# Kernel optimization log

Measured on AMD Instinct MI355X. Metric: run time of the kernel, lower is better.

## Reference

```python
import jax, jax.numpy as jnp
import numpy as np

S, B, L = 64, 32, 64          # seq_len (messages), batch (convs), max tokens per message
V, D = 32000, 300             # vocab, embedding dim
H = 512                       # hidden_dim; per-direction message hidden = H//2
F = 16                        # num_game_features
Hh = H // 2


def lstm_dir(x, mask, Wih, Whh, b, reverse=False):
    """Masked (packed-equivalent) LSTM. x:(T,N,D), mask:(T,N) bool.
    Returns h:(T,N,H) with zeros at invalid steps (matches pad_packed_sequence)."""
    if reverse:
        x, mask = x[::-1], mask[::-1]
    N = x.shape[1]
    Hd = Whh.shape[1]
    xg = jnp.einsum('tnd,gd->tng', x, Wih) + b  # (T,N,4H) input gates precomputed

    def step(carry, inp):
        h, c = carry
        xg_t, m = inp
        g = xg_t + h @ Whh.T
        i, f, gg, o = jnp.split(g, 4, axis=-1)
        c_new = jax.nn.sigmoid(f) * c + jax.nn.sigmoid(i) * jnp.tanh(gg)
        h_new = jax.nn.sigmoid(o) * jnp.tanh(c_new)
        m = m[:, None]
        return (jnp.where(m, h_new, h), jnp.where(m, c_new, c)), jnp.where(m, h_new, 0.0)

    init = (jnp.zeros((N, Hd), x.dtype), jnp.zeros((N, Hd), x.dtype))
    _, hs = jax.lax.scan(step, init, (xg, mask))
    if reverse:
        hs = hs[::-1]
    return hs


def setup_inputs() -> dict:
    key = jax.random.key(0)
    ks = jax.random.split(key, 16)
    s = 1.0 / np.sqrt(Hh)
    sc = 1.0 / np.sqrt(H)
    inp = {
        'messages': jax.random.randint(ks[0], (S, B, L), 0, V),
        'game_features': jax.random.normal(ks[1], (S, B, F), jnp.float32),
        'conv_lengths': jax.random.randint(ks[2], (B,), 1, S + 1),
        'E': jax.random.normal(ks[3], (V, D), jnp.float32) * 0.1,  # frozen embedding
        # message bi-LSTM (forward dir)
        'Wih_f': jax.random.uniform(ks[4], (4 * Hh, D), jnp.float32, -s, s),
        'Whh_f': jax.random.uniform(ks[5], (4 * Hh, Hh), jnp.float32, -s, s),
        'b_f': jax.random.uniform(ks[6], (4 * Hh,), jnp.float32, -s, s),
        # message bi-LSTM (backward dir)
        'Wih_b': jax.random.uniform(ks[7], (4 * Hh, D), jnp.float32, -s, s),
        'Whh_b': jax.random.uniform(ks[8], (4 * Hh, Hh), jnp.float32, -s, s),
        'b_b': jax.random.uniform(ks[9], (4 * Hh,), jnp.float32, -s, s),
        # conversation LSTM
        'Wih_c': jax.random.uniform(ks[10], (4 * H, H), jnp.float32, -sc, sc),
        'Whh_c': jax.random.uniform(ks[11], (4 * H, H), jnp.float32, -sc, sc),
        'b_c': jax.random.uniform(ks[12], (4 * H,), jnp.float32, -sc, sc),
        # classifier
        'Wc': jax.random.uniform(ks[13], (H + F,), jnp.float32, -sc, sc),
        'bc': jax.random.uniform(ks[14], (), jnp.float32, -sc, sc),
    }
    return inp


def reference(messages, game_features, conv_lengths, E, Wih_f, Whh_f, b_f,
              Wih_b, Whh_b, b_b, Wih_c, Whh_c, b_c, Wc, bc):
    # ---- message level: all S*B messages in one batched bi-LSTM pass ----
    flat = messages.reshape(S * B, L)                       # (N, L)
    emb = E[flat]                                           # (N, L, D)
    msg_len = jnp.maximum((flat != 0).sum(1), 1)            # clamp(min=1)
    tmask = jnp.arange(L)[:, None] < msg_len[None, :]       # (L, N)
    x = emb.transpose(1, 0, 2)                              # (L, N, D) time-major
    h_fwd = lstm_dir(x, tmask, Wih_f, Whh_f, b_f, reverse=False)
    h_bwd = lstm_dir(x, tmask, Wih_b, Whh_b, b_b, reverse=True)
    h = jnp.concatenate([h_fwd, h_bwd], axis=-1)            # (L, N, H); zeros at pad
    enc = h.max(axis=0)                                     # maxpool incl. zero pads (torch semantics)
    enc = enc.reshape(S, B, H)
    # ---- conversation level ----
    cmask = jnp.arange(S)[:, None] < conv_lengths[None, :]  # (S, B)
    conv_out = lstm_dir(enc, cmask, Wih_c, Whh_c, b_c)      # (S, B, H), zeros past length
    # dropout is identity at inference
    combined = jnp.concatenate([conv_out, game_features], axis=2)  # (S, B, H+F)
    logits = combined @ Wc + bc                             # (S, B)
    return logits
```

## Files before the change

### kernel.cpp

```cpp
#include <hip/hip_runtime.h>
#include <cmath>

#define S_DIM 64
#define B_DIM 32
#define L_DIM 64
#define NMSG  2048
#define D_DIM 300
#define HH    256
#define HC    512
#define F_DIM 16
#define VOCAB 32000

#define OFF_XGV   0u
#define OFF_WHH   32768000u
#define OFF_WPI   33030144u
#define OFF_WCI   33357824u
#define OFF_WCR   33882112u
#define OFF_ENCB  34406400u
#define OFF_HCONV 34930688u
#define OFF_CCONV 34938880u
#define OFF_CO    34955264u
#define OFF_MLEN  36003840u

typedef __attribute__((ext_vector_type(8))) short s8v;
typedef __attribute__((ext_vector_type(4))) float f4v;
#define MFMA(a,b,c) __builtin_amdgcn_mfma_f32_16x16x32_bf16((a),(b),(c),0,0,0)

__device__ __forceinline__ unsigned short f2bf(float x) {
    unsigned u = __float_as_uint(x);
    return (unsigned short)((u + 0x7FFFu + ((u >> 16) & 1u)) >> 16);
}
__device__ __forceinline__ float bf2f(unsigned short u) {
    return __uint_as_float(((unsigned)u) << 16);
}
__device__ __forceinline__ float sigm(float x) { return 1.0f / (1.0f + __expf(-x)); }
__device__ __forceinline__ float tanh_f(float x) { return 1.0f - 2.0f / (1.0f + __expf(2.0f * x)); }

__device__ __forceinline__ void gload16(const unsigned short* g, unsigned short* l) {
    __builtin_amdgcn_global_load_lds(
        (const __attribute__((address_space(1))) unsigned int*)g,
        (__attribute__((address_space(3))) unsigned int*)l, 16, 0, 0);
}

__global__ __launch_bounds__(256) void pack_whh(
    const float* __restrict__ Whh_f, const float* __restrict__ Whh_b,
    unsigned short* __restrict__ Wp)
{
    int nt = blockIdx.x, dir = blockIdx.y;
    const float* W = dir ? Whh_b : Whh_f;
    int tid = threadIdx.x, lane = tid & 63, ktq = tid >> 6;
    int n = nt * 16 + (lane & 15);
    int kb = (lane >> 4) * 8;
    #pragma unroll
    for (int pass = 0; pass < 2; ++pass) {
        int kt = ktq + pass * 4;
        int k0 = kt * 32 + kb;
        unsigned short tmp[8];
        #pragma unroll
        for (int u = 0; u < 8; ++u) tmp[u] = f2bf(W[(size_t)n * HH + k0 + u]);
        *(uint4*)(Wp + (size_t)dir * 262144 + ((size_t)(nt * 8 + kt)) * 512 + lane * 8) = *(uint4*)tmp;
    }
}

__global__ __launch_bounds__(256) void pack_wih(
    const float* __restrict__ Wih_f, const float* __restrict__ Wih_b,
    unsigned short* __restrict__ wpi)
{
    int nt = blockIdx.x, dir = blockIdx.y;
    const float* W = dir ? Wih_b : Wih_f;
    int tid = threadIdx.x, lane = tid & 63, ktq = tid >> 6;
    int n = nt * 16 + (lane & 15);
    int kb = (lane >> 4) * 8;
    for (int kt = ktq; kt < 10; kt += 4) {
        int k0 = kt * 32 + kb;
        unsigned short tmp[8];
        #pragma unroll
        for (int u = 0; u < 8; ++u) {
            int k = k0 + u;
            tmp[u] = (k < D_DIM) ? f2bf(W[(size_t)n * D_DIM + k]) : (unsigned short)0;
        }
        *(uint4*)(wpi + (size_t)dir * 327680 + ((size_t)(nt * 10 + kt)) * 512 + lane * 8) = *(uint4*)tmp;
    }
}

__global__ __launch_bounds__(256) void pack_whc(
    const float* __restrict__ Wih_c, const float* __restrict__ Whh_c,
    unsigned short* __restrict__ whci, unsigned short* __restrict__ whcr)
{
    int nt = blockIdx.x, which = blockIdx.y;
    const float* W = which ? Whh_c : Wih_c;
    unsigned short* dst = which ? whcr : whci;
    int tid = threadIdx.x, lane = tid & 63;
    int row = nt * 16 + (lane & 15);
    int kb = (lane >> 4) * 8;
    for (int kt = tid >> 6; kt < 16; kt += 4) {
        int k0 = kt * 32 + kb;
        unsigned short tmp[8];
        #pragma unroll
        for (int u = 0; u < 8; ++u) tmp[u] = f2bf(W[(size_t)row * HC + k0 + u]);
        *(uint4*)(dst + ((size_t)(nt * 16 + kt)) * 512 + lane * 8) = *(uint4*)tmp;
    }
}

__global__ __launch_bounds__(256) void msg_len_kernel(const int* __restrict__ msgs,
                                                      int* __restrict__ mlen) {
    int n = blockIdx.x * 256 + threadIdx.x;
    if (n >= NMSG) return;
    int cnt = 0;
    #pragma unroll 8
    for (int l = 0; l < L_DIM; ++l) cnt += (msgs[n * L_DIM + l] != 0);
    mlen[n] = max(cnt, 1);
}

__global__ __launch_bounds__(256) void init_conv(float* __restrict__ ws) {
    unsigned i = blockIdx.x * 256u + threadIdx.x;
    if (i < 24576u) ws[OFF_HCONV + i] = 0.0f;
}

#define EROW 328
__global__ __launch_bounds__(256) void xg_gemm(
    const float* __restrict__ E,
    const float* __restrict__ b_f, const float* __restrict__ b_b,
    const unsigned short* __restrict__ wpi,
    unsigned short* __restrict__ xgv)
{
    __shared__ __align__(16) unsigned short e_lds[32 * EROW];
    __shared__ __align__(16) float gbuf[32 * 264];
    const int w0 = blockIdx.x * 32;
    const int n0 = blockIdx.y * 256;
    const int dirb = n0 >> 10;
    const int nb = n0 & 1023;
    const float* bias = dirb ? b_b : b_f;

    const int tid = threadIdx.x, lane = tid & 63, wv = tid >> 6;
    const int l15 = lane & 15, kg = lane >> 4;

    for (int i = tid; i < 32 * 320; i += 256) {
        int r = i / 320, k = i - r * 320;
        float v = (k < D_DIM) ? E[(size_t)(w0 + r) * D_DIM + k] : 0.0f;
        e_lds[r * EROW + k] = f2bf(v);
    }
    __syncthreads();

    const unsigned short* wb = wpi + (size_t)dirb * 327680;
    const f4v zf = {0.0f, 0.0f, 0.0f, 0.0f};
    f4v acc[2][4];
    #pragma unroll
    for (int m = 0; m < 2; ++m)
        #pragma unroll
        for (int q = 0; q < 4; ++q) acc[m][q] = zf;

    for (int kt = 0; kt < 10; ++kt) {
        s8v a0 = *(const s8v*)&e_lds[l15 * EROW + kt * 32 + kg * 8];
        s8v a1 = *(const s8v*)&e_lds[(16 + l15) * EROW + kt * 32 + kg * 8];
        #pragma unroll
        for (int q = 0; q < 4; ++q) {
            int ntg = (nb >> 4) + wv * 4 + q;
            s8v b = *(const s8v*)(wb + ((size_t)(ntg * 10 + kt)) * 512 + lane * 8);
            acc[0][q] = MFMA(a0, b, acc[0][q]);
            acc[1][q] = MFMA(a1, b, acc[1][q]);
        }
    }

    #pragma unroll
    for (int q = 0; q < 4; ++q) {
        int col = (wv * 4 + q) * 16 + l15;
        float bv = bias[nb + col];
        #pragma unroll
        for (int m = 0; m < 2; ++m)
            #pragma unroll
            for (int r = 0; r < 4; ++r)
                gbuf[(m * 16 + kg * 4 + r) * 264 + col] = acc[m][q][r] + bv;
    }
    __syncthreads();
    {
        int row = tid >> 3, ch = tid & 7;
        unsigned short tmp[32];
        #pragma unroll
        for (int cc = 0; cc < 32; ++cc) tmp[cc] = f2bf(gbuf[row * 264 + ch * 32 + cc]);
        uint4* dst = (uint4*)(xgv + ((size_t)dirb * VOCAB + w0 + row) * 1024 + nb + ch * 32);
        const uint4* s4 = (const uint4*)tmp;
        #pragma unroll
        for (int u = 0; u < 4; ++u) dst[u] = s4[u];
    }
}

#define XGS  1032
#define HROW 264
__global__ __launch_bounds__(512, 2) void word_lstm(
    const int* __restrict__ msgs, const int* __restrict__ mlen,
    const unsigned short* __restrict__ xgv,
    const unsigned short* __restrict__ whh,
    unsigned short* __restrict__ enc_bf)
{
    __shared__ __align__(16) unsigned short xg_lds[2][16 * XGS];
    __shared__ __align__(16) unsigned short h_lds[16 * HROW];
    __shared__ int tok_s[16 * 64];
    __shared__ int len_s[16];

    const int mg = blockIdx.x >> 1, dir = blockIdx.x & 1;
    const int tid = threadIdx.x, lane = tid & 63, wv = tid >> 6;
    const int l15 = lane & 15, kg = lane >> 4;

    for (int i = tid; i < 16 * 64; i += 512) tok_s[i] = msgs[mg * 1024 + i];
    if (tid < 16) len_s[tid] = mlen[mg * 16 + tid];
    for (int i = tid; i < 16 * HROW; i += 512) h_lds[i] = 0;
    __syncthreads();

    const unsigned short* xv = xgv + (size_t)dir * VOCAB * 1024;
    const unsigned short* wb = whh + (size_t)dir * 262144;

    s8v bw[4][8];
    #pragma unroll
    for (int i = 0; i < 4; ++i)
        #pragma unroll
        for (int kt = 0; kt < 8; ++kt)
            bw[i][kt] = *(const s8v*)(wb + ((size_t)((((i >> 1) * 16 + wv * 2 + (i & 1)) * 8) + kt)) * 512 + lane * 8);
    #pragma unroll
    for (int i = 0; i < 4; ++i)
        #pragma unroll
        for (int kt = 0; kt < 8; ++kt)
            asm volatile("" : "+v"(bw[i][kt]));

    int lens[4];
    #pragma unroll
    for (int r = 0; r < 4; ++r) lens[r] = len_s[kg * 4 + r];

    int bmax = 1;
    #pragma unroll
    for (int i = 0; i < 16; ++i) bmax = max(bmax, len_s[i]);

    float c_st[2][4], rm[2][4];
    #pragma unroll
    for (int q = 0; q < 2; ++q)
        #pragma unroll
        for (int r = 0; r < 4; ++r) { c_st[q][r] = 0.0f; rm[q][r] = -INFINITY; }

    #pragma unroll
    for (int rr = 0; rr < 2; ++rr) {
        int row = wv * 2 + rr;
        int tt = dir ? (len_s[row] - 1) : 0;
        if (tt < 0) tt = 0;
        const unsigned short* src = xv + (size_t)tok_s[row * 64 + tt] * 1024 + lane * 8;
        gload16(src,       &xg_lds[0][row * XGS]);
        gload16(src + 512, &xg_lds[0][row * XGS + 512]);
    }

    for (int t = 0; t < bmax; ++t) {
        __syncthreads();
        const int buf = t & 1;

        if (t + 1 < bmax) {
            #pragma unroll
            for (int rr = 0; rr < 2; ++rr) {
                int row = wv * 2 + rr;
                int tn = t + 1;
                int tt = dir ? (len_s[row] - 1 - tn) : tn;
                if (tt < 0) tt = 0;
                const unsigned short* src = xv + (size_t)tok_s[row * 64 + tt] * 1024 + lane * 8;
                gload16(src,       &xg_lds[buf ^ 1][row * XGS]);
                gload16(src + 512, &xg_lds[buf ^ 1][row * XGS + 512]);
            }
        }

        f4v acc[2][4];
        #pragma unroll
        for (int q = 0; q < 2; ++q)
            #pragma unroll
            for (int g = 0; g < 4; ++g) {
                f4v v;
                #pragma unroll
                for (int r = 0; r < 4; ++r)
                    v[r] = bf2f(xg_lds[buf][(kg * 4 + r) * XGS + g * 256 + wv * 32 + q * 16 + l15]);
                acc[q][g] = v;
            }

        #pragma unroll
        for (int kt = 0; kt < 8; ++kt) {
            s8v a = *(const s8v*)&h_lds[l15 * HROW + kt * 32 + kg * 8];
            #pragma unroll
            for (int i = 0; i < 4; ++i)
                acc[i & 1][i >> 1] = MFMA(a, bw[i][kt], acc[i & 1][i >> 1]);
            #pragma unroll
            for (int i = 4; i < 8; ++i) {
                s8v b = *(const s8v*)(wb + ((size_t)((((i >> 1) * 16 + wv * 2 + (i & 1)) * 8) + kt)) * 512 + lane * 8);
                acc[i & 1][i >> 1] = MFMA(a, b, acc[i & 1][i >> 1]);
            }
        }

        float hv[2][4];
        #pragma unroll
        for (int q = 0; q < 2; ++q)
            #pragma unroll
            for (int r = 0; r < 4; ++r) {
                float gi = acc[q][0][r], gf = acc[q][1][r], gc = acc[q][2][r], go = acc[q][3][r];
                float cn = sigm(gf) * c_st[q][r] + sigm(gi) * tanh_f(gc);
                float hn = sigm(go) * tanh_f(cn);
                hv[q][r] = hn;
                if (t < lens[r]) { c_st[q][r] = cn; rm[q][r] = fmaxf(rm[q][r], hn); }
            }
        __syncthreads();
        #pragma unroll
        for (int q = 0; q < 2; ++q)
            #pragma unroll
            for (int r = 0; r < 4; ++r)
                if (t < lens[r])
                    h_lds[(kg * 4 + r) * HROW + wv * 32 + q * 16 + l15] = f2bf(hv[q][r]);
    }

    #pragma unroll
    for (int q = 0; q < 2; ++q)
        #pragma unroll
        for (int r = 0; r < 4; ++r) {
            float v = rm[q][r];
            if (lens[r] < 64) v = fmaxf(v, 0.0f);
            enc_bf[(size_t)(mg * 16 + kg * 4 + r) * HC + dir * HH + wv * 32 + q * 16 + l15] = f2bf(v);
        }
}

#define CROW 520
__global__ __launch_bounds__(256) void xgc_gemm(
    const unsigned short* __restrict__ enc_bf,
    const unsigned short* __restrict__ whci,
    const float* __restrict__ b_c,
    unsigned short* __restrict__ xgc)
{
    __shared__ __align__(16) unsigned short e_lds[32 * CROW];
    const int m0 = blockIdx.x * 32;
    const int n0 = blockIdx.y * 256;
    const int tid = threadIdx.x, lane = tid & 63, wv = tid >> 6;
    const int l15 = lane & 15, kg = lane >> 4;

    for (int i = tid; i < 2048; i += 256) {
        int row = i >> 6, u4 = i & 63;
        ((uint4*)&e_lds[row * CROW])[u4] = ((const uint4*)(enc_bf + (size_t)(m0 + row) * HC))[u4];
    }
    __syncthreads();

    const f4v zf = {0.0f, 0.0f, 0.0f, 0.0f};
    f4v acc[2][4];
    #pragma unroll
    for (int m = 0; m < 2; ++m)
        #pragma unroll
        for (int q = 0; q < 4; ++q) acc[m][q] = zf;

    for (int kt = 0; kt < 16; ++kt) {
        s8v a0 = *(const s8v*)&e_lds[l15 * CROW + kt * 32 + kg * 8];
        s8v a1 = *(const s8v*)&e_lds[(16 + l15) * CROW + kt * 32 + kg * 8];
        #pragma unroll
        for (int q = 0; q < 4; ++q) {
            int nt = (n0 >> 4) + wv * 4 + q;
            s8v b = *(const s8v*)(whci + ((size_t)(nt * 16 + kt)) * 512 + lane * 8);
            acc[0][q] = MFMA(a0, b, acc[0][q]);
            acc[1][q] = MFMA(a1, b, acc[1][q]);
        }
    }

    #pragma unroll
    for (int q = 0; q < 4; ++q) {
        int col = n0 + (wv * 4 + q) * 16 + l15;
        float bv = b_c[col];
        #pragma unroll
        for (int m = 0; m < 2; ++m)
            #pragma unroll
            for (int r = 0; r < 4; ++r)
                xgc[(size_t)(m0 + m * 16 + kg * 4 + r) * 2048 + col] = f2bf(acc[m][q][r] + bv);
    }
}

__global__ __launch_bounds__(256) void conv_step(
    const unsigned short* __restrict__ whcr,
    const unsigned short* __restrict__ xgc,
    const int* __restrict__ conv_len,
    unsigned short* __restrict__ h_bf,
    float* __restrict__ c_ws,
    float* __restrict__ co,
    int s)
{
    __shared__ __align__(16) unsigned short xh[32 * CROW];
    __shared__ float gbuf[4][32][16];

    const int tid = threadIdx.x, jb = blockIdx.x;
    const int lane = tid & 63, g = tid >> 6;
    const int l15 = lane & 15, kg = lane >> 4;

    for (int i = tid; i < 2048; i += 256) {
        int row = i >> 6, u4 = i & 63;
        ((uint4*)&xh[row * CROW])[u4] = ((const uint4*)(h_bf + (size_t)row * HC))[u4];
    }
    __syncthreads();

    const int col = g * 512 + jb * 16 + l15;
    f4v acc0, acc1;
    #pragma unroll
    for (int r = 0; r < 4; ++r) {
        acc0[r] = bf2f(xgc[(size_t)(s * B_DIM + kg * 4 + r) * 2048 + col]);
        acc1[r] = bf2f(xgc[(size_t)(s * B_DIM + 16 + kg * 4 + r) * 2048 + col]);
    }

    const int nt = g * 32 + jb;
    for (int kt = 0; kt < 16; ++kt) {
        s8v a0 = *(const s8v*)&xh[l15 * CROW + kt * 32 + kg * 8];
        s8v a1 = *(const s8v*)&xh[(16 + l15) * CROW + kt * 32 + kg * 8];
        s8v b  = *(const s8v*)(whcr + ((size_t)(nt * 16 + kt)) * 512 + lane * 8);
        acc0 = MFMA(a0, b, acc0);
        acc1 = MFMA(a1, b, acc1);
    }

    #pragma unroll
    for (int r = 0; r < 4; ++r) {
        gbuf[g][kg * 4 + r][l15]      = acc0[r];
        gbuf[g][16 + kg * 4 + r][l15] = acc1[r];
    }
    __syncthreads();

    #pragma unroll
    for (int u = 0; u < 2; ++u) {
        int cell = tid + 256 * u;
        int b = cell >> 4, jj = cell & 15;
        int j = jb * 16 + jj;
        bool valid = s < conv_len[b];
        float g_i = gbuf[0][b][jj], g_f = gbuf[1][b][jj];
        float g_c = gbuf[2][b][jj], g_o = gbuf[3][b][jj];
        float cold = c_ws[b * HC + j];
        float cn = sigm(g_f) * cold + sigm(g_i) * tanh_f(g_c);
        float hn = sigm(g_o) * tanh_f(cn);
        float outv = 0.0f;
        if (valid) {
            c_ws[b * HC + j] = cn;
            h_bf[b * HC + j] = f2bf(hn);
            outv = hn;
        }
        co[((size_t)s * B_DIM + b) * HC + j] = outv;
    }
}

__global__ __launch_bounds__(256) void logits_kernel(
    const float* __restrict__ gfeat, const float* __restrict__ Wc, const float* __restrict__ bc,
    const float* __restrict__ co, float* __restrict__ out)
{
    int o = blockIdx.x * 4 + (threadIdx.x >> 6);
    int lane = threadIdx.x & 63;
    const float* row = co + (size_t)o * HC;
    float sum = 0.0f;
    #pragma unroll
    for (int u = 0; u < 8; ++u) sum += row[lane + 64 * u] * Wc[lane + 64 * u];
    if (lane < F_DIM) sum += gfeat[o * F_DIM + lane] * Wc[HC + lane];
    #pragma unroll
    for (int off = 32; off > 0; off >>= 1) sum += __shfl_down(sum, off, 64);
    if (lane == 0) out[o] = sum + bc[0];
}

extern "C" void kernel_launch(void* const* d_in, const int* in_sizes, int n_in,
                              void* d_out, int out_size, void* d_ws, size_t ws_size,
                              hipStream_t stream) {
    const int*   msgs    = (const int*)  d_in[0];
    const float* gfeat   = (const float*)d_in[1];
    const int*   convlen = (const int*)  d_in[2];
    const float* E       = (const float*)d_in[3];
    const float* Wih_f   = (const float*)d_in[4];
    const float* Whh_f   = (const float*)d_in[5];
    const float* b_f     = (const float*)d_in[6];
    const float* Wih_b   = (const float*)d_in[7];
    const float* Whh_b   = (const float*)d_in[8];
    const float* b_b     = (const float*)d_in[9];
    const float* Wih_c   = (const float*)d_in[10];
    const float* Whh_c   = (const float*)d_in[11];
    const float* b_c     = (const float*)d_in[12];
    const float* Wc      = (const float*)d_in[13];
    const float* bc      = (const float*)d_in[14];
    float* out = (float*)d_out;
    float* ws  = (float*)d_ws;

    unsigned short* xgv    = (unsigned short*)(ws + OFF_XGV);
    unsigned short* xgc    = (unsigned short*)(ws + OFF_XGV);
    unsigned short* whh    = (unsigned short*)(ws + OFF_WHH);
    unsigned short* wpi    = (unsigned short*)(ws + OFF_WPI);
    unsigned short* whci   = (unsigned short*)(ws + OFF_WCI);
    unsigned short* whcr   = (unsigned short*)(ws + OFF_WCR);
    unsigned short* enc_bf = (unsigned short*)(ws + OFF_ENCB);
    unsigned short* h_bf   = (unsigned short*)(ws + OFF_HCONV);
    float*          c_ws   = ws + OFF_CCONV;
    float*          co     = ws + OFF_CO;
    int*            mlen   = (int*)(ws + OFF_MLEN);

    pack_whh<<<dim3(64, 2), 256, 0, stream>>>(Whh_f, Whh_b, whh);
    pack_wih<<<dim3(64, 2), 256, 0, stream>>>(Wih_f, Wih_b, wpi);
    pack_whc<<<dim3(128, 2), 256, 0, stream>>>(Wih_c, Whh_c, whci, whcr);
    msg_len_kernel<<<NMSG / 256, 256, 0, stream>>>(msgs, mlen);
    init_conv<<<96, 256, 0, stream>>>(ws);
    xg_gemm<<<dim3(1000, 8), 256, 0, stream>>>(E, b_f, b_b, wpi, xgv);

    word_lstm<<<256, 512, 0, stream>>>(msgs, mlen, xgv, whh, enc_bf);

    xgc_gemm<<<dim3(64, 8), 256, 0, stream>>>(enc_bf, whci, b_c, xgc);

    for (int s = 0; s < S_DIM; ++s)
        conv_step<<<32, 256, 0, stream>>>(whcr, xgc, convlen, h_bf, c_ws, co, s);

    logits_kernel<<<NMSG / 4, 256, 0, stream>>>(gfeat, Wc, bc, co, out);
}
```

Before: 1.333 ms.

## Double-buffer LSTM hidden state and repack gate layouts for vector loads

The word-level LSTM now double-buffers the hidden state in LDS, which drops the second barrier in each timestep. Masked rows carry their last bf16 hidden value forward through a register. The Whh pack and the xg GEMM output are reordered into a per-wave, gate-interleaved layout. This lets each thread fetch its four gate inputs with single 16-byte LDS reads and stream its recurrent weights with contiguous loads. The register-resident weight half (bw) is removed, so all recurrent weights are now read from global/L2 every step. That frees registers but adds memory traffic per timestep.

Result: faster. 1.215 ms (-8.9%).

```diff
diff --git a/kernel.cpp b/kernel.cpp
--- a/kernel.cpp
+++ b/kernel.cpp
@@ -46,19 +46,20 @@
     const float* __restrict__ Whh_f, const float* __restrict__ Whh_b,
     unsigned short* __restrict__ Wp)
 {
-    int nt = blockIdx.x, dir = blockIdx.y;
+    int wv = blockIdx.x >> 3, kt = blockIdx.x & 7, dir = blockIdx.y;
     const float* W = dir ? Whh_b : Whh_f;
-    int tid = threadIdx.x, lane = tid & 63, ktq = tid >> 6;
-    int n = nt * 16 + (lane & 15);
-    int kb = (lane >> 4) * 8;
-    #pragma unroll
-    for (int pass = 0; pass < 2; ++pass) {
-        int kt = ktq + pass * 4;
-        int k0 = kt * 32 + kb;
+    int tid = threadIdx.x, lane = tid & 63, iq = tid >> 6;
+    int n_l = lane & 15;
+    int k0 = kt * 32 + (lane >> 4) * 8;
+    #pragma unroll
+    for (int ii = 0; ii < 2; ++ii) {
+        int i = iq * 2 + ii;
+        int nt = (i >> 1) * 16 + wv * 2 + (i & 1);
+        int n = nt * 16 + n_l;
         unsigned short tmp[8];
         #pragma unroll
         for (int u = 0; u < 8; ++u) tmp[u] = f2bf(W[(size_t)n * HH + k0 + u]);
-        *(uint4*)(Wp + (size_t)dir * 262144 + ((size_t)(nt * 8 + kt)) * 512 + lane * 8) = *(uint4*)tmp;
+        *(uint4*)(Wp + ((size_t)((dir * 8 + wv) * 8 + kt) * 8 + i) * 512 + lane * 8) = *(uint4*)tmp;
     }
 }
 
@@ -125,11 +126,9 @@
     unsigned short* __restrict__ xgv)
 {
     __shared__ __align__(16) unsigned short e_lds[32 * EROW];
-    __shared__ __align__(16) float gbuf[32 * 264];
     const int w0 = blockIdx.x * 32;
-    const int n0 = blockIdx.y * 256;
-    const int dirb = n0 >> 10;
-    const int nb = n0 & 1023;
+    const int dirb = blockIdx.y >> 2;
+    const int jt = blockIdx.y & 3;
     const float* bias = dirb ? b_b : b_f;
 
     const int tid = threadIdx.x, lane = tid & 63, wv = tid >> 6;
@@ -148,41 +147,35 @@
     #pragma unroll
     for (int m = 0; m < 2; ++m)
         #pragma unroll
-        for (int q = 0; q < 4; ++q) acc[m][q] = zf;
+        for (int g = 0; g < 4; ++g) acc[m][g] = zf;
 
     for (int kt = 0; kt < 10; ++kt) {
         s8v a0 = *(const s8v*)&e_lds[l15 * EROW + kt * 32 + kg * 8];
         s8v a1 = *(const s8v*)&e_lds[(16 + l15) * EROW + kt * 32 + kg * 8];
         #pragma unroll
-        for (int q = 0; q < 4; ++q) {
-            int ntg = (nb >> 4) + wv * 4 + q;
-            s8v b = *(const s8v*)(wb + ((size_t)(ntg * 10 + kt)) * 512 + lane * 8);
-            acc[0][q] = MFMA(a0, b, acc[0][q]);
-            acc[1][q] = MFMA(a1, b, acc[1][q]);
-        }
-    }
-
-    #pragma unroll
-    for (int q = 0; q < 4; ++q) {
-        int col = (wv * 4 + q) * 16 + l15;
-        float bv = bias[nb + col];
-        #pragma unroll
-        for (int m = 0; m < 2; ++m)
-            #pragma unroll
-            for (int r = 0; r < 4; ++r)
-                gbuf[(m * 16 + kg * 4 + r) * 264 + col] = acc[m][q][r] + bv;
-    }
-    __syncthreads();
-    {
-        int row = tid >> 3, ch = tid & 7;
-        unsigned short tmp[32];
-        #pragma unroll
-        for (int cc = 0; cc < 32; ++cc) tmp[cc] = f2bf(gbuf[row * 264 + ch * 32 + cc]);
-        uint4* dst = (uint4*)(xgv + ((size_t)dirb * VOCAB + w0 + row) * 1024 + nb + ch * 32);
-        const uint4* s4 = (const uint4*)tmp;
-        #pragma unroll
-        for (int u = 0; u < 4; ++u) dst[u] = s4[u];
-    }
+        for (int g = 0; g < 4; ++g) {
+            int nt = g * 16 + jt * 4 + wv;
+            s8v b = *(const s8v*)(wb + ((size_t)(nt * 10 + kt)) * 512 + lane * 8);
+            acc[0][g] = MFMA(a0, b, acc[0][g]);
+            acc[1][g] = MFMA(a1, b, acc[1][g]);
+        }
+    }
+
+    const int j = jt * 64 + wv * 16 + l15;
+    float bv[4];
+    #pragma unroll
+    for (int g = 0; g < 4; ++g) bv[g] = bias[g * 256 + j];
+    const int colp = (jt * 2 + (wv >> 1)) * 128 + l15 * 8 + (wv & 1) * 4;
+    #pragma unroll
+    for (int m = 0; m < 2; ++m)
+        #pragma unroll
+        for (int r = 0; r < 4; ++r) {
+            int w = w0 + m * 16 + kg * 4 + r;
+            unsigned short t4[4];
+            #pragma unroll
+            for (int g = 0; g < 4; ++g) t4[g] = f2bf(acc[m][g][r] + bv[g]);
+            *(uint2*)(xgv + ((size_t)dirb * VOCAB + w) * 1024 + colp) = *(uint2*)t4;
+        }
 }
 
 #define XGS  1032
@@ -194,7 +187,7 @@
     unsigned short* __restrict__ enc_bf)
 {
     __shared__ __align__(16) unsigned short xg_lds[2][16 * XGS];
-    __shared__ __align__(16) unsigned short h_lds[16 * HROW];
+    __shared__ __align__(16) unsigned short h_lds[2][16 * HROW];
     __shared__ int tok_s[16 * 64];
     __shared__ int len_s[16];
 
@@ -204,23 +197,15 @@
 
     for (int i = tid; i < 16 * 64; i += 512) tok_s[i] = msgs[mg * 1024 + i];
     if (tid < 16) len_s[tid] = mlen[mg * 16 + tid];
-    for (int i = tid; i < 16 * HROW; i += 512) h_lds[i] = 0;
+    for (int i = tid; i < 2 * 16 * HROW; i += 512) h_lds[0][i] = 0;
     __syncthreads();
 
     const unsigned short* xv = xgv + (size_t)dir * VOCAB * 1024;
-    const unsigned short* wb = whh + (size_t)dir * 262144;
-
-    s8v bw[4][8];
-    #pragma unroll
-    for (int i = 0; i < 4; ++i)
-        #pragma unroll
-        for (int kt = 0; kt < 8; ++kt)
-            bw[i][kt] = *(const s8v*)(wb + ((size_t)((((i >> 1) * 16 + wv * 2 + (i & 1)) * 8) + kt)) * 512 + lane * 8);
-    #pragma unroll
-    for (int i = 0; i < 4; ++i)
-        #pragma unroll
-        for (int kt = 0; kt < 8; ++kt)
-            asm volatile("" : "+v"(bw[i][kt]));
+
+    const unsigned short* wbase = whh + (size_t)(dir * 8 + wv) * 32768 + lane * 8;
+    const unsigned short* bp[16];
+    #pragma unroll
+    for (int jj = 0; jj < 16; ++jj) bp[jj] = wbase + jj * 2048;
 
     int lens[4];
     #pragma unroll
@@ -231,10 +216,11 @@
     for (int i = 0; i < 16; ++i) bmax = max(bmax, len_s[i]);
 
     float c_st[2][4], rm[2][4];
+    unsigned short hbf[2][4];
     #pragma unroll
     for (int q = 0; q < 2; ++q)
         #pragma unroll
-        for (int r = 0; r < 4; ++r) { c_st[q][r] = 0.0f; rm[q][r] = -INFINITY; }
+        for (int r = 0; r < 4; ++r) { c_st[q][r] = 0.0f; rm[q][r] = -INFINITY; hbf[q][r] = 0; }
 
     #pragma unroll
     for (int rr = 0; rr < 2; ++rr) {
@@ -249,6 +235,7 @@
     for (int t = 0; t < bmax; ++t) {
         __syncthreads();
         const int buf = t & 1;
+        const int hbuf = t & 1;
 
         if (t + 1 < bmax) {
             #pragma unroll
@@ -264,31 +251,38 @@
         }
 
         f4v acc[2][4];
-        #pragma unroll
-        for (int q = 0; q < 2; ++q)
-            #pragma unroll
-            for (int g = 0; g < 4; ++g) {
-                f4v v;
+        {
+            s8v v8[4];
+            #pragma unroll
+            for (int r = 0; r < 4; ++r)
+                v8[r] = *(const s8v*)&xg_lds[buf][(kg * 4 + r) * XGS + wv * 128 + l15 * 8];
+            #pragma unroll
+            for (int q = 0; q < 2; ++q)
                 #pragma unroll
-                for (int r = 0; r < 4; ++r)
-                    v[r] = bf2f(xg_lds[buf][(kg * 4 + r) * XGS + g * 256 + wv * 32 + q * 16 + l15]);
-                acc[q][g] = v;
-            }
+                for (int g = 0; g < 4; ++g) {
+                    f4v v;
+                    #pragma unroll
+                    for (int r = 0; r < 4; ++r)
+                        v[r] = bf2f((unsigned short)v8[r][q * 4 + g]);
+                    acc[q][g] = v;
+                }
+        }
 
         #pragma unroll
         for (int kt = 0; kt < 8; ++kt) {
-            s8v a = *(const s8v*)&h_lds[l15 * HROW + kt * 32 + kg * 8];
-            #pragma unroll
-            for (int i = 0; i < 4; ++i)
-                acc[i & 1][i >> 1] = MFMA(a, bw[i][kt], acc[i & 1][i >> 1]);
-            #pragma unroll
-            for (int i = 4; i < 8; ++i) {
-                s8v b = *(const s8v*)(wb + ((size_t)((((i >> 1) * 16 + wv * 2 + (i & 1)) * 8) + kt)) * 512 + lane * 8);
-                acc[i & 1][i >> 1] = MFMA(a, b, acc[i & 1][i >> 1]);
-            }
-        }
-
-        float hv[2][4];
+            s8v a = *(const s8v*)&h_lds[hbuf][l15 * HROW + kt * 32 + kg * 8];
+            const unsigned short* pA = bp[kt * 2];
+            const unsigned short* pB = bp[kt * 2 + 1];
+            acc[0][0] = MFMA(a, *(const s8v*)(pA),        acc[0][0]);
+            acc[1][0] = MFMA(a, *(const s8v*)(pA + 512),  acc[1][0]);
+            acc[0][1] = MFMA(a, *(const s8v*)(pA + 1024), acc[0][1]);
+            acc[1][1] = MFMA(a, *(const s8v*)(pA + 1536), acc[1][1]);
+            acc[0][2] = MFMA(a, *(const s8v*)(pB),        acc[0][2]);
+            acc[1][2] = MFMA(a, *(const s8v*)(pB + 512),  acc[1][2]);
+            acc[0][3] = MFMA(a, *(const s8v*)(pB + 1024), acc[0][3]);
+            acc[1][3] = MFMA(a, *(const s8v*)(pB + 1536), acc[1][3]);
+        }
+
         #pragma unroll
         for (int q = 0; q < 2; ++q)
             #pragma unroll
@@ -296,16 +290,13 @@
                 float gi = acc[q][0][r], gf = acc[q][1][r], gc = acc[q][2][r], go = acc[q][3][r];
                 float cn = sigm(gf) * c_st[q][r] + sigm(gi) * tanh_f(gc);
                 float hn = sigm(go) * tanh_f(cn);
-                hv[q][r] = hn;
-                if (t < lens[r]) { c_st[q][r] = cn; rm[q][r] = fmaxf(rm[q][r], hn); }
+                if (t < lens[r]) {
+                    c_st[q][r] = cn;
+                    rm[q][r] = fmaxf(rm[q][r], hn);
+                    hbf[q][r] = f2bf(hn);
+                }
+                h_lds[hbuf ^ 1][(kg * 4 + r) * HROW + wv * 32 + q * 16 + l15] = hbf[q][r];
             }
-        __syncthreads();
-        #pragma unroll
-        for (int q = 0; q < 2; ++q)
-            #pragma unroll
-            for (int r = 0; r < 4; ++r)
-                if (t < lens[r])
-                    h_lds[(kg * 4 + r) * HROW + wv * 32 + q * 16 + l15] = f2bf(hv[q][r]);
     }
 
     #pragma unroll
```
